# Optimization experiments

Measured on AMD Instinct MI355X. Metric: run time of the kernel, lower is better.

## Reference

```python
import jax, jax.numpy as jnp
import numpy as np
from jax import lax

B = 65536

def _conv3(x, w, b):
    # x: [B,Cin,H,W], w: [Cout,Cin,3,3] (OIHW), SAME padding, stride 1
    y = lax.conv_general_dilated(x, w, (1, 1), 'SAME',
                                 dimension_numbers=('NCHW', 'OIHW', 'NCHW'))
    return y + b[None, :, None, None]

def _gru_cell(x, h, wu, bu, wr, br, wo, bo):
    s = jnp.concatenate([x, h], axis=1)
    update = jax.nn.sigmoid(_conv3(s, wu, bu))
    reset = jax.nn.sigmoid(_conv3(s, wr, br))
    out = jnp.tanh(_conv3(jnp.concatenate([x, h * reset], axis=1), wo, bo))
    return h * (1.0 - update) + out * update

def _mk_cell_params(key, cin, ch):
    ks = jax.random.split(key, 6)
    fan = (cin + ch) * 9
    sc = 1.0 / np.sqrt(fan)
    p = {}
    for i, g in enumerate(['u', 'r', 'o']):
        p['w' + g] = jax.random.normal(ks[2 * i], (ch, cin + ch, 3, 3), jnp.float32) * sc
        p['b' + g] = jax.random.normal(ks[2 * i + 1], (ch,), jnp.float32) * sc
    return p

def setup_inputs() -> dict:
    key = jax.random.key(0)
    k_in, k1, k2, k3, kd1, kd2 = jax.random.split(key, 6)
    inputs = jax.random.normal(k_in, (B, 1, 3, 3), jnp.float32)
    p1 = _mk_cell_params(k1, 1, 32)
    p2 = _mk_cell_params(k2, 32, 64)
    p3 = _mk_cell_params(k3, 64, 16)
    wd = jax.random.normal(kd1, (9, 16 * 3 * 3), jnp.float32) * (1.0 / 12.0)
    bd = jax.random.normal(kd2, (9,), jnp.float32) * (1.0 / 12.0)
    out = {'inputs': inputs, 'wd': wd, 'bd': bd}
    for i, p in enumerate([p1, p2, p3], start=1):
        for k, v in p.items():
            out[f'{k[0]}{i}{k[1]}'] = v  # e.g. w1u, b1u
    return out

def reference(inputs, wd, bd,
              w1u, b1u, w1r, b1r, w1o, b1o,
              w2u, b2u, w2r, b2r, w2o, b2o,
              w3u, b3u, w3r, b3r, w3o, b3o):
    b = inputs.shape[0]
    h1 = jnp.zeros((b, 32, 3, 3), inputs.dtype)
    h2 = jnp.zeros((b, 64, 3, 3), inputs.dtype)
    h3 = jnp.zeros((b, 16, 3, 3), inputs.dtype)
    x1 = _gru_cell(inputs, h1, w1u, b1u, w1r, b1r, w1o, b1o)
    x2 = _gru_cell(x1, h2, w2u, b2u, w2r, b2r, w2o, b2o)
    x3 = _gru_cell(x2, h3, w3u, b3u, w3r, b3r, w3o, b3o)
    out = x3.reshape(b, -1) @ wd.T + bd
    return (out, x1, x2, x3)
```

## Files before the change

### kernel.cpp

```cpp
#include <hip/hip_runtime.h>

#define BATCH 65536

typedef __attribute__((ext_vector_type(8))) short bf16x8;
typedef __attribute__((ext_vector_type(4))) float f32x4;

__device__ __forceinline__ unsigned short f2bf(float f) {
  unsigned int u = __float_as_uint(f);
  u += 0x7fffu + ((u >> 16) & 1u);
  return (unsigned short)(u >> 16);
}
__device__ __forceinline__ unsigned pack_trunc(float lo, float hi) {
  return __builtin_amdgcn_perm(__float_as_uint(hi), __float_as_uint(lo), 0x07060302u);
}

__device__ __forceinline__ float gru_act(float u, float o) {
  u = fmaxf(u, -60.0f);
  o = fmaxf(o, -30.0f);
  float a  = __expf(-u);
  float a2 = __expf(-2.0f * o);
  return (1.0f - a2) * __builtin_amdgcn_rcpf((1.0f + a) * (1.0f + a2));
}

__device__ __forceinline__ float conv_tap(const float* __restrict__ w, int co, int ci,
                                          int p, int q, int CINTOT) {
  int pi = p / 3, pj = p % 3, qi = q / 3, qj = q % 3;
  int di = qi - pi + 1, dj = qj - pj + 1;
  if ((unsigned)di < 3u && (unsigned)dj < 3u)
    return w[((co * CINTOT + ci) * 3 + di) * 3 + dj];
  return 0.0f;
}

__global__ void build_bt(const float* __restrict__ wu, const float* __restrict__ wo,
                         unsigned short* __restrict__ BT, int COUT, int CINX, int CINTOT) {
  int NG = COUT * 9, K = CINX * 9;
  int total = 2 * NG * K;
  int e = blockIdx.x * 256 + threadIdx.x;
  if (e >= total) return;
  int g = e / (NG * K);
  int rem = e - g * (NG * K);
  int n = rem / K, k = rem - n * K;
  BT[e] = f2bf(conv_tap(g ? wo : wu, n / 9, k / 9, n % 9, k % 9, CINTOT));
}

__global__ void build_a1(const float* __restrict__ wu, const float* __restrict__ wo,
                         float* __restrict__ A1) {
  int e = blockIdx.x * 256 + threadIdx.x;
  if (e >= 5184) return;
  int g = e / 2592;
  int rem = e - g * 2592;
  int q = rem / 288, c = rem - q * 288;
  A1[e] = conv_tap(g ? wo : wu, c / 9, 0, c % 9, q, 33);
}

#define OFF_X1L 0
#define OFF_X3L 0
#define OFF_WL 20480
#define OFF_BLB 25664
#define OFF_BL 40960
#define OFF_XL 65536
#define OFF_AL 65536
#define SMEM_BYTES 69632

__global__ __launch_bounds__(512, 4) void megafused(
    const float* __restrict__ xin, const float* __restrict__ A1,
    const float* __restrict__ b1u, const float* __restrict__ b1o,
    const unsigned short* __restrict__ BT2,
    const float* __restrict__ b2u, const float* __restrict__ b2o,
    const unsigned short* __restrict__ BT3,
    const float* __restrict__ b3u, const float* __restrict__ b3o,
    const float* __restrict__ wd, const float* __restrict__ bd,
    float* __restrict__ x1, float* __restrict__ x2,
    float* __restrict__ x3, float* __restrict__ out) {
  __shared__ __align__(16) char smem[SMEM_BYTES];
  char* x1l = smem + OFF_X1L;
  char* Bl = smem + OFF_BL;
  char* Al = smem + OFF_AL;
  unsigned short* x3l = (unsigned short*)(smem + OFF_X3L);
  float* xl = (float*)(smem + OFF_XL);
  float* wl = (float*)(smem + OFF_WL);
  float* blb = (float*)(smem + OFF_BLB);

  const int tid = threadIdx.x;
  const int lane = tid & 63;
  const int wid = tid >> 6;
  const int lrow = lane & 15;
  const int jc = (lane >> 4) & 3;
  const int mh = wid >> 2;
  const int cg = wid & 3;
  const int r0 = blockIdx.x * 64;
  const int srow = tid >> 2, spart = tid & 3;

  unsigned toffB2[3];
  char* wB2[3];
#pragma unroll
  for (int ci = 0; ci < 3; ++ci) {
    int row = ci * 128 + srow;
    int bg = (row < 192) ? row : (384 + row);
    toffB2[ci] = (unsigned)bg * 288u + spart * 8;
    wB2[ci] = Bl + row * 64 + ((spart ^ ((row >> 1) & 3)) << 4);
  }

  for (int c = tid; c < 576; c += 512) xl[(c / 9) * 12 + (c % 9)] = xin[(size_t)r0 * 9 + c];
  __syncthreads();

  bf16x8 pf[3];
#pragma unroll
  for (int ci = 0; ci < 3; ++ci) pf[ci] = *(const bf16x8*)(BT2 + toffB2[ci]);

  for (int uu = 0; uu < 3; ++uu) {
    int u = tid + (uu << 9);
    if (u < 1152) {
      int c = u >> 2, rq = u & 3;
      float au[9], ao[9];
#pragma unroll
      for (int q = 0; q < 9; ++q) {
        au[q] = A1[q * 288 + c];
        ao[q] = A1[2592 + q * 288 + c];
      }
      float bU = b1u[c / 9], bO = b1o[c / 9];
      const int cbase = c >> 3, cb = (c & 7) * 2;
#pragma unroll 4
      for (int i = 0; i < 16; ++i) {
        int r = (rq << 4) + i;
        const float4 xv0 = *(const float4*)&xl[r * 12];
        const float4 xv1 = *(const float4*)&xl[r * 12 + 4];
        const float x8 = xl[r * 12 + 8];
        float uacc = bU, oacc = bO;
        uacc = fmaf(au[0], xv0.x, uacc); oacc = fmaf(ao[0], xv0.x, oacc);
        uacc = fmaf(au[1], xv0.y, uacc); oacc = fmaf(ao[1], xv0.y, oacc);
        uacc = fmaf(au[2], xv0.z, uacc); oacc = fmaf(ao[2], xv0.z, oacc);
        uacc = fmaf(au[3], xv0.w, uacc); oacc = fmaf(ao[3], xv0.w, oacc);
        uacc = fmaf(au[4], xv1.x, uacc); oacc = fmaf(ao[4], xv1.x, oacc);
        uacc = fmaf(au[5], xv1.y, uacc); oacc = fmaf(ao[5], xv1.y, oacc);
        uacc = fmaf(au[6], xv1.z, uacc); oacc = fmaf(ao[6], xv1.z, oacc);
        uacc = fmaf(au[7], xv1.w, uacc); oacc = fmaf(ao[7], xv1.w, oacc);
        uacc = fmaf(au[8], x8, uacc);    oacc = fmaf(ao[8], x8, oacc);
        float v = gru_act(uacc, oacc);
        x1[(size_t)(r0 + r) * 288 + c] = v;
        *(unsigned short*)(x1l + r * 640 + ((cbase ^ (r & 7)) << 4) + cb) =
            (unsigned short)(__float_as_uint(v) >> 16);
      }
    }
  }

  {
    const char* rB[2][3];
#pragma unroll
    for (int g = 0; g < 2; ++g)
#pragma unroll
      for (int f = 0; f < 3; ++f) {
        int rb = g * 192 + (cg * 3 + f) * 16 + lrow;
        rB[g][f] = Bl + rb * 64 + ((jc ^ ((rb >> 1) & 3)) << 4);
      }
    const char* aBase[2];
    int aXor[2];
#pragma unroll
    for (int m = 0; m < 2; ++m) {
      int row = mh * 32 + m * 16 + lrow;
      aBase[m] = x1l + row * 640;
      aXor[m] = row & 7;
    }

    f32x4 acc[2][2][3] = {};
    for (int s = 0; s < 27; ++s) {
      const int kt = s - (s / 9) * 9;
#pragma unroll
      for (int ci = 0; ci < 3; ++ci) *(bf16x8*)wB2[ci] = pf[ci];
      __syncthreads();
      if (s < 26) {
        int ns = s + 1;
        unsigned uoff = (unsigned)(ns / 9) * 55296u + (unsigned)(ns % 9) * 32u;
#pragma unroll
        for (int ci = 0; ci < 3; ++ci)
          pf[ci] = *(const bf16x8*)(BT2 + uoff + toffB2[ci]);
      }
      bf16x8 af[2];
      const int c8 = kt * 4 + jc;
#pragma unroll
      for (int m = 0; m < 2; ++m)
        af[m] = *(const bf16x8*)(aBase[m] + ((c8 ^ aXor[m]) << 4));
      bf16x8 bfr[2][3];
#pragma unroll
      for (int g = 0; g < 2; ++g)
#pragma unroll
        for (int f = 0; f < 3; ++f) bfr[g][f] = *(const bf16x8*)rB[g][f];
#pragma unroll
      for (int m = 0; m < 2; ++m)
#pragma unroll
        for (int g = 0; g < 2; ++g)
#pragma unroll
          for (int f = 0; f < 3; ++f)
            acc[m][g][f] = __builtin_amdgcn_mfma_f32_16x16x32_bf16(
                af[m], bfr[g][f], acc[m][g][f], 0, 0, 0);
      if (kt == 8) {
        const int n0 = (s / 9) * 192;
#pragma unroll
        for (int m = 0; m < 2; ++m)
#pragma unroll
          for (int f = 0; f < 3; ++f) {
            int n = n0 + (cg * 3 + f) * 16 + lrow;
            float bU = b2u[n / 9], bO = b2o[n / 9];
            f32x4 u = acc[m][0][f], o = acc[m][1][f];
#pragma unroll
            for (int t = 0; t < 4; ++t) {
              int r = r0 + mh * 32 + m * 16 + jc * 4 + t;
              x2[(size_t)r * 576 + n] = gru_act(u[t] + bU, o[t] + bO);
            }
            acc[m][0][f] = (f32x4){0.f, 0.f, 0.f, 0.f};
            acc[m][1][f] = (f32x4){0.f, 0.f, 0.f, 0.f};
          }
      }
      __syncthreads();
    }
  }

  {
    unsigned toffB3[3];
    char* wB3[3];
    bool vB3[3];
#pragma unroll
    for (int ci = 0; ci < 3; ++ci) {
      int row = ci * 128 + srow;
      int g = row >= 192;
      int nloc = row - (g ? 192 : 0);
      vB3[ci] = (nloc < 144);
      toffB3[ci] = (unsigned)((g ? 144 : 0) + nloc) * 576u + spart * 8;
      wB3[ci] = Bl + row * 64 + ((spart ^ ((row >> 1) & 3)) << 4);
    }
    const float* pA = x2 + (size_t)(r0 + (tid >> 2)) * 576 + spart * 8;
    char* wAl = Al + (tid >> 2) * 64 + ((spart ^ (((tid >> 2) >> 1) & 3)) << 4);

    float4 pa0 = {}, pa1 = {};
    if (tid < 256) {
      pa0 = *(const float4*)pA;
      pa1 = *(const float4*)(pA + 4);
    }
    bf16x8 pb[3];
#pragma unroll
    for (int ci = 0; ci < 3; ++ci)
      pb[ci] = vB3[ci] ? *(const bf16x8*)(BT3 + toffB3[ci])
                       : (bf16x8){0, 0, 0, 0, 0, 0, 0, 0};

    for (int c = tid; c < 1296; c += 512) wl[c] = wd[c];
    if (tid < 9) blb[tid] = bd[tid];

    const char* rB3[2][3];
#pragma unroll
    for (int g = 0; g < 2; ++g)
#pragma unroll
      for (int f = 0; f < 3; ++f) {
        int rb = g * 192 + (cg * 3 + f) * 16 + lrow;
        rB3[g][f] = Bl + rb * 64 + ((jc ^ ((rb >> 1) & 3)) << 4);
      }
    const char* rA3[2];
#pragma unroll
    for (int m = 0; m < 2; ++m) {
      int row = mh * 32 + m * 16 + lrow;
      rA3[m] = Al + row * 64 + ((jc ^ ((row >> 1) & 3)) << 4);
    }

    f32x4 acc[2][2][3] = {};
    for (int kt = 0; kt < 18; ++kt) {
      if (tid < 256) {
        uint4 h;
        h.x = pack_trunc(pa0.x, pa0.y);
        h.y = pack_trunc(pa0.z, pa0.w);
        h.z = pack_trunc(pa1.x, pa1.y);
        h.w = pack_trunc(pa1.z, pa1.w);
        *(uint4*)wAl = h;
      }
#pragma unroll
      for (int ci = 0; ci < 3; ++ci) *(bf16x8*)wB3[ci] = pb[ci];
      __syncthreads();
      if (kt < 17) {
        if (tid < 256) {
          const float* gp = pA + (kt + 1) * 32;
          pa0 = *(const float4*)gp;
          pa1 = *(const float4*)(gp + 4);
        }
        unsigned uoff = (unsigned)(kt + 1) * 32u;
#pragma unroll
        for (int ci = 0; ci < 3; ++ci)
          if (vB3[ci]) pb[ci] = *(const bf16x8*)(BT3 + uoff + toffB3[ci]);
      }
      bf16x8 af[2];
#pragma unroll
      for (int m = 0; m < 2; ++m) af[m] = *(const bf16x8*)rA3[m];
      bf16x8 bfr[2][3];
#pragma unroll
      for (int g = 0; g < 2; ++g)
#pragma unroll
        for (int f = 0; f < 3; ++f) bfr[g][f] = *(const bf16x8*)rB3[g][f];
#pragma unroll
      for (int m = 0; m < 2; ++m)
#pragma unroll
        for (int g = 0; g < 2; ++g)
#pragma unroll
          for (int f = 0; f < 3; ++f)
            acc[m][g][f] = __builtin_amdgcn_mfma_f32_16x16x32_bf16(
                af[m], bfr[g][f], acc[m][g][f], 0, 0, 0);
      __syncthreads();
    }
    if (cg < 3) {
#pragma unroll
      for (int m = 0; m < 2; ++m)
#pragma unroll
        for (int f = 0; f < 3; ++f) {
          int n = (cg * 3 + f) * 16 + lrow;
          float bU = b3u[n / 9], bO = b3o[n / 9];
          f32x4 u = acc[m][0][f], o = acc[m][1][f];
#pragma unroll
          for (int t = 0; t < 4; ++t) {
            int r = mh * 32 + m * 16 + jc * 4 + t;
            float v = gru_act(u[t] + bU, o[t] + bO);
            x3[(size_t)(r0 + r) * 144 + n] = v;
            x3l[r * 146 + n] = (unsigned short)(__float_as_uint(v) >> 16);
          }
        }
    }
  }
  __syncthreads();

  {
    int row = lane;
    int j = wid;
    float s = blb[j];
    for (int k = 0; k < 144; k += 2) {
      unsigned pr = *(const unsigned*)&x3l[row * 146 + k];
      float v0 = __uint_as_float(pr << 16);
      float v1 = __uint_as_float(pr & 0xffff0000u);
      const float2 w0 = *(const float2*)&wl[j * 144 + k];
      s = fmaf(v0, w0.x, s);
      s = fmaf(v1, w0.y, s);
    }
    out[(size_t)(r0 + row) * 9 + j] = s;
    if (tid < 64) {
      float s8 = blb[8];
      for (int k = 0; k < 144; k += 2) {
        unsigned pr = *(const unsigned*)&x3l[row * 146 + k];
        float v0 = __uint_as_float(pr << 16);
        float v1 = __uint_as_float(pr & 0xffff0000u);
        const float2 w0 = *(const float2*)&wl[8 * 144 + k];
        s8 = fmaf(v0, w0.x, s8);
        s8 = fmaf(v1, w0.y, s8);
      }
      out[(size_t)(r0 + row) * 9 + 8] = s8;
    }
  }
}

extern "C" void kernel_launch(void* const* d_in, const int* in_sizes, int n_in,
                              void* d_out, int out_size, void* d_ws, size_t ws_size,
                              hipStream_t stream) {
  const float* inputs = (const float*)d_in[0];
  const float* wd  = (const float*)d_in[1];
  const float* bd  = (const float*)d_in[2];
  const float* w1u = (const float*)d_in[3];
  const float* b1u = (const float*)d_in[4];
  const float* w1o = (const float*)d_in[7];
  const float* b1o = (const float*)d_in[8];
  const float* w2u = (const float*)d_in[9];
  const float* b2u = (const float*)d_in[10];
  const float* w2o = (const float*)d_in[13];
  const float* b2o = (const float*)d_in[14];
  const float* w3u = (const float*)d_in[15];
  const float* b3u = (const float*)d_in[16];
  const float* w3o = (const float*)d_in[19];
  const float* b3o = (const float*)d_in[20];

  float* out = (float*)d_out;
  float* x1 = out + (size_t)BATCH * 9;
  float* x2 = x1 + (size_t)BATCH * 288;
  float* x3 = x2 + (size_t)BATCH * 576;

  unsigned short* BT2 = (unsigned short*)d_ws;
  unsigned short* BT3 = BT2 + 331776;
  float* A1 = (float*)((char*)d_ws + 995328);

  build_bt<<<1296, 256, 0, stream>>>(w2u, w2o, BT2, 64, 32, 96);
  build_bt<<<648, 256, 0, stream>>>(w3u, w3o, BT3, 16, 64, 80);
  build_a1<<<21, 256, 0, stream>>>(w1u, w1o, A1);

  megafused<<<BATCH / 64, 512, 0, stream>>>(inputs, A1, b1u, b1o, BT2, b2u, b2o,
                                            BT3, b3u, b3o, wd, bd, x1, x2, x3, out);
}
```

Measured before the change: 163.5 us.

## Double-buffer LDS tiles for layer 2/3 GEMMs with one barrier per step

Splits the weight and activation LDS tiles into two buffers, so the next k-step's tile is written while the current one is consumed. This drops one of the two __syncthreads per iteration, replacing it with a custom s_waitcnt plus s_barrier, and prefetches global data two steps ahead. LDS use grows to about 100KB, so launch bounds fall from 4 to 2 blocks per CU, which cuts occupancy and latency hiding. The layer-1 input row stride also changes from 12 to 13 floats, which alters the LDS bank mapping for those loads.

```diff
diff --git a/kernel.cpp b/kernel.cpp
--- a/kernel.cpp
+++ b/kernel.cpp
@@ -20,6 +20,13 @@
   float a  = __expf(-u);
   float a2 = __expf(-2.0f * o);
   return (1.0f - a2) * __builtin_amdgcn_rcpf((1.0f + a) * (1.0f + a2));
+}
+
+__device__ __forceinline__ void bar_lds() {
+  asm volatile("s_waitcnt lgkmcnt(0)" ::: "memory");
+  __builtin_amdgcn_sched_barrier(0);
+  __builtin_amdgcn_s_barrier();
+  __builtin_amdgcn_sched_barrier(0);
 }
 
 __device__ __forceinline__ float conv_tap(const float* __restrict__ w, int co, int ci,
@@ -58,11 +65,13 @@
 #define OFF_WL 20480
 #define OFF_BLB 25664
 #define OFF_BL 40960
-#define OFF_XL 65536
-#define OFF_AL 65536
-#define SMEM_BYTES 69632
-
-__global__ __launch_bounds__(512, 4) void megafused(
+#define BL_STRIDE 24576
+#define OFF_AL 90112
+#define AL_STRIDE 4096
+#define OFF_XL 98304
+#define SMEM_BYTES 101632
+
+__global__ __launch_bounds__(512, 2) void megafused(
     const float* __restrict__ xin, const float* __restrict__ A1,
     const float* __restrict__ b1u, const float* __restrict__ b1o,
     const unsigned short* __restrict__ BT2,
@@ -92,16 +101,16 @@
   const int srow = tid >> 2, spart = tid & 3;
 
   unsigned toffB2[3];
-  char* wB2[3];
+  int wOffB2[3];
 #pragma unroll
   for (int ci = 0; ci < 3; ++ci) {
     int row = ci * 128 + srow;
     int bg = (row < 192) ? row : (384 + row);
     toffB2[ci] = (unsigned)bg * 288u + spart * 8;
-    wB2[ci] = Bl + row * 64 + ((spart ^ ((row >> 1) & 3)) << 4);
+    wOffB2[ci] = row * 64 + ((spart ^ ((row >> 1) & 3)) << 4);
   }
 
-  for (int c = tid; c < 576; c += 512) xl[(c / 9) * 12 + (c % 9)] = xin[(size_t)r0 * 9 + c];
+  for (int c = tid; c < 576; c += 512) xl[(c / 9) * 13 + (c % 9)] = xin[(size_t)r0 * 9 + c];
   __syncthreads();
 
   bf16x8 pf[3];
@@ -123,9 +132,9 @@
 #pragma unroll 4
       for (int i = 0; i < 16; ++i) {
         int r = (rq << 4) + i;
-        const float4 xv0 = *(const float4*)&xl[r * 12];
-        const float4 xv1 = *(const float4*)&xl[r * 12 + 4];
-        const float x8 = xl[r * 12 + 8];
+        const float4 xv0 = *(const float4*)&xl[r * 13];
+        const float4 xv1 = *(const float4*)&xl[r * 13 + 4];
+        const float x8 = xl[r * 13 + 8];
         float uacc = bU, oacc = bO;
         uacc = fmaf(au[0], xv0.x, uacc); oacc = fmaf(ao[0], xv0.x, oacc);
         uacc = fmaf(au[1], xv0.y, uacc); oacc = fmaf(ao[1], xv0.y, oacc);
@@ -145,13 +154,13 @@
   }
 
   {
-    const char* rB[2][3];
+    int rBoff[2][3];
 #pragma unroll
     for (int g = 0; g < 2; ++g)
 #pragma unroll
       for (int f = 0; f < 3; ++f) {
         int rb = g * 192 + (cg * 3 + f) * 16 + lrow;
-        rB[g][f] = Bl + rb * 64 + ((jc ^ ((rb >> 1) & 3)) << 4);
+        rBoff[g][f] = rb * 64 + ((jc ^ ((rb >> 1) & 3)) << 4);
       }
     const char* aBase[2];
     int aXor[2];
@@ -162,19 +171,16 @@
       aXor[m] = row & 7;
     }
 
+#pragma unroll
+    for (int ci = 0; ci < 3; ++ci) *(bf16x8*)(Bl + wOffB2[ci]) = pf[ci];
+#pragma unroll
+    for (int ci = 0; ci < 3; ++ci) pf[ci] = *(const bf16x8*)(BT2 + 32u + toffB2[ci]);
+    bar_lds();
+
     f32x4 acc[2][2][3] = {};
     for (int s = 0; s < 27; ++s) {
       const int kt = s - (s / 9) * 9;
-#pragma unroll
-      for (int ci = 0; ci < 3; ++ci) *(bf16x8*)wB2[ci] = pf[ci];
-      __syncthreads();
-      if (s < 26) {
-        int ns = s + 1;
-        unsigned uoff = (unsigned)(ns / 9) * 55296u + (unsigned)(ns % 9) * 32u;
-#pragma unroll
-        for (int ci = 0; ci < 3; ++ci)
-          pf[ci] = *(const bf16x8*)(BT2 + uoff + toffB2[ci]);
-      }
+      const int bsel = (s & 1) * BL_STRIDE;
       bf16x8 af[2];
       const int c8 = kt * 4 + jc;
 #pragma unroll
@@ -184,7 +190,8 @@
 #pragma unroll
       for (int g = 0; g < 2; ++g)
 #pragma unroll
-        for (int f = 0; f < 3; ++f) bfr[g][f] = *(const bf16x8*)rB[g][f];
+        for (int f = 0; f < 3; ++f)
+          bfr[g][f] = *(const bf16x8*)(Bl + bsel + rBoff[g][f]);
 #pragma unroll
       for (int m = 0; m < 2; ++m)
 #pragma unroll
@@ -211,13 +218,27 @@
             acc[m][1][f] = (f32x4){0.f, 0.f, 0.f, 0.f};
           }
       }
-      __syncthreads();
+      if (s < 26) {
+        const int wsel = ((s + 1) & 1) * BL_STRIDE;
+#pragma unroll
+        for (int ci = 0; ci < 3; ++ci)
+          *(bf16x8*)(Bl + wsel + wOffB2[ci]) = pf[ci];
+        if (s < 25) {
+          int ns = s + 2;
+          unsigned uoff = (unsigned)(ns / 9) * 55296u + (unsigned)(ns % 9) * 32u;
+#pragma unroll
+          for (int ci = 0; ci < 3; ++ci)
+            pf[ci] = *(const bf16x8*)(BT2 + uoff + toffB2[ci]);
+        }
+        bar_lds();
+      }
     }
   }
+  __syncthreads();
 
   {
     unsigned toffB3[3];
-    char* wB3[3];
+    int wOffB3[3];
     bool vB3[3];
 #pragma unroll
     for (int ci = 0; ci < 3; ++ci) {
@@ -226,10 +247,10 @@
       int nloc = row - (g ? 192 : 0);
       vB3[ci] = (nloc < 144);
       toffB3[ci] = (unsigned)((g ? 144 : 0) + nloc) * 576u + spart * 8;
-      wB3[ci] = Bl + row * 64 + ((spart ^ ((row >> 1) & 3)) << 4);
+      wOffB3[ci] = row * 64 + ((spart ^ ((row >> 1) & 3)) << 4);
     }
     const float* pA = x2 + (size_t)(r0 + (tid >> 2)) * 576 + spart * 8;
-    char* wAl = Al + (tid >> 2) * 64 + ((spart ^ (((tid >> 2) >> 1) & 3)) << 4);
+    const int wAloff = (tid >> 2) * 64 + ((spart ^ (((tid >> 2) >> 1) & 3)) << 4);
 
     float4 pa0 = {}, pa1 = {};
     if (tid < 256) {
@@ -245,53 +266,53 @@
     for (int c = tid; c < 1296; c += 512) wl[c] = wd[c];
     if (tid < 9) blb[tid] = bd[tid];
 
-    const char* rB3[2][3];
+    int rBoff3[2][3];
 #pragma unroll
     for (int g = 0; g < 2; ++g)
 #pragma unroll
       for (int f = 0; f < 3; ++f) {
         int rb = g * 192 + (cg * 3 + f) * 16 + lrow;
-        rB3[g][f] = Bl + rb * 64 + ((jc ^ ((rb >> 1) & 3)) << 4);
-      }
-    const char* rA3[2];
+        rBoff3[g][f] = rb * 64 + ((jc ^ ((rb >> 1) & 3)) << 4);
+      }
+    int rAoff3[2];
 #pragma unroll
     for (int m = 0; m < 2; ++m) {
       int row = mh * 32 + m * 16 + lrow;
-      rA3[m] = Al + row * 64 + ((jc ^ ((row >> 1) & 3)) << 4);
-    }
+      rAoff3[m] = row * 64 + ((jc ^ ((row >> 1) & 3)) << 4);
+    }
+
+    if (tid < 256) {
+      uint4 h;
+      h.x = pack_trunc(pa0.x, pa0.y);
+      h.y = pack_trunc(pa0.z, pa0.w);
+      h.z = pack_trunc(pa1.x, pa1.y);
+      h.w = pack_trunc(pa1.z, pa1.w);
+      *(uint4*)(Al + wAloff) = h;
+    }
+#pragma unroll
+    for (int ci = 0; ci < 3; ++ci) *(bf16x8*)(Bl + wOffB3[ci]) = pb[ci];
+    if (tid < 256) {
+      pa0 = *(const float4*)(pA + 32);
+      pa1 = *(const float4*)(pA + 36);
+    }
+#pragma unroll
+    for (int ci = 0; ci < 3; ++ci)
+      if (vB3[ci]) pb[ci] = *(const bf16x8*)(BT3 + 32u + toffB3[ci]);
+    bar_lds();
 
     f32x4 acc[2][2][3] = {};
     for (int kt = 0; kt < 18; ++kt) {
-      if (tid < 256) {
-        uint4 h;
-        h.x = pack_trunc(pa0.x, pa0.y);
-        h.y = pack_trunc(pa0.z, pa0.w);
-        h.z = pack_trunc(pa1.x, pa1.y);
-        h.w = pack_trunc(pa1.z, pa1.w);
-        *(uint4*)wAl = h;
-      }
-#pragma unroll
-      for (int ci = 0; ci < 3; ++ci) *(bf16x8*)wB3[ci] = pb[ci];
-      __syncthreads();
-      if (kt < 17) {
-        if (tid < 256) {
-          const float* gp = pA + (kt + 1) * 32;
-          pa0 = *(const float4*)gp;
-          pa1 = *(const float4*)(gp + 4);
-        }
-        unsigned uoff = (unsigned)(kt + 1) * 32u;
-#pragma unroll
-        for (int ci = 0; ci < 3; ++ci)
-          if (vB3[ci]) pb[ci] = *(const bf16x8*)(BT3 + uoff + toffB3[ci]);
-      }
+      const int bsel = (kt & 1) * BL_STRIDE;
+      const int asel = (kt & 1) * AL_STRIDE;
       bf16x8 af[2];
 #pragma unroll
-      for (int m = 0; m < 2; ++m) af[m] = *(const bf16x8*)rA3[m];
+      for (int m = 0; m < 2; ++m) af[m] = *(const bf16x8*)(Al + asel + rAoff3[m]);
       bf16x8 bfr[2][3];
 #pragma unroll
       for (int g = 0; g < 2; ++g)
 #pragma unroll
-        for (int f = 0; f < 3; ++f) bfr[g][f] = *(const bf16x8*)rB3[g][f];
+        for (int f = 0; f < 3; ++f)
+          bfr[g][f] = *(const bf16x8*)(Bl + bsel + rBoff3[g][f]);
 #pragma unroll
       for (int m = 0; m < 2; ++m)
 #pragma unroll
@@ -300,7 +321,33 @@
           for (int f = 0; f < 3; ++f)
             acc[m][g][f] = __builtin_amdgcn_mfma_f32_16x16x32_bf16(
                 af[m], bfr[g][f], acc[m][g][f], 0, 0, 0);
-      __syncthreads();
+      if (kt < 17) {
+        const int wbsel = ((kt + 1) & 1) * BL_STRIDE;
+        const int wasel = ((kt + 1) & 1) * AL_STRIDE;
+        if (tid < 256) {
+          uint4 h;
+          h.x = pack_trunc(pa0.x, pa0.y);
+          h.y = pack_trunc(pa0.z, pa0.w);
+          h.z = pack_trunc(pa1.x, pa1.y);
+          h.w = pack_trunc(pa1.z, pa1.w);
+          *(uint4*)(Al + wasel + wAloff) = h;
+        }
+#pragma unroll
+        for (int ci = 0; ci < 3; ++ci)
+          *(bf16x8*)(Bl + wbsel + wOffB3[ci]) = pb[ci];
+        if (kt < 16) {
+          if (tid < 256) {
+            const float* gp = pA + (kt + 2) * 32;
+            pa0 = *(const float4*)gp;
+            pa1 = *(const float4*)(gp + 4);
+          }
+          unsigned uoff = (unsigned)(kt + 2) * 32u;
+#pragma unroll
+          for (int ci = 0; ci < 3; ++ci)
+            if (vB3[ci]) pb[ci] = *(const bf16x8*)(BT3 + uoff + toffB3[ci]);
+        }
+        bar_lds();
+      }
     }
     if (cg < 3) {
 #pragma unroll
```

Measured after the change: 217.1 us. 32.8% more time.

## Load GEMM weight fragments directly from global into registers, dropping LDS staging

Applied to the files above, without the earlier changes.

Layer-2 and layer-3 MFMA loops no longer stage B weight tiles through shared memory. Each wave now loads its own bf16 fragments straight from global into a double-buffered register set, and layer 3 reads and packs its x2 A-operand directly from global. This removes the two __syncthreads per k-step and shrinks shared memory from about 68 KB to about 43 KB, which may allow more resident blocks; the xl row stride also changes to 13 to avoid bank conflicts. The cost is redundant global/L2 traffic, since waves sharing a column group each fetch the same weights, and more register pressure from the double buffers and full unrolling.

```diff
diff --git a/kernel.cpp b/kernel.cpp
--- a/kernel.cpp
+++ b/kernel.cpp
@@ -57,10 +57,8 @@
 #define OFF_X3L 0
 #define OFF_WL 20480
 #define OFF_BLB 25664
-#define OFF_BL 40960
-#define OFF_XL 65536
-#define OFF_AL 65536
-#define SMEM_BYTES 69632
+#define OFF_XL 40960
+#define SMEM_BYTES 44288
 
 __global__ __launch_bounds__(512, 4) void megafused(
     const float* __restrict__ xin, const float* __restrict__ A1,
@@ -74,8 +72,6 @@
     float* __restrict__ x3, float* __restrict__ out) {
   __shared__ __align__(16) char smem[SMEM_BYTES];
   char* x1l = smem + OFF_X1L;
-  char* Bl = smem + OFF_BL;
-  char* Al = smem + OFF_AL;
   unsigned short* x3l = (unsigned short*)(smem + OFF_X3L);
   float* xl = (float*)(smem + OFF_XL);
   float* wl = (float*)(smem + OFF_WL);
@@ -89,24 +85,22 @@
   const int mh = wid >> 2;
   const int cg = wid & 3;
   const int r0 = blockIdx.x * 64;
-  const int srow = tid >> 2, spart = tid & 3;
-
-  unsigned toffB2[3];
-  char* wB2[3];
-#pragma unroll
-  for (int ci = 0; ci < 3; ++ci) {
-    int row = ci * 128 + srow;
-    int bg = (row < 192) ? row : (384 + row);
-    toffB2[ci] = (unsigned)bg * 288u + spart * 8;
-    wB2[ci] = Bl + row * 64 + ((spart ^ ((row >> 1) & 3)) << 4);
-  }
-
-  for (int c = tid; c < 576; c += 512) xl[(c / 9) * 12 + (c % 9)] = xin[(size_t)r0 * 9 + c];
+
+  unsigned bvoff[3];
+#pragma unroll
+  for (int f = 0; f < 3; ++f)
+    bvoff[f] = (unsigned)(((cg * 3 + f) * 16 + lrow) * 576 + jc * 16);
+  const char* BT2b = (const char*)BT2;
+
+  for (int c = tid; c < 576; c += 512) xl[(c / 9) * 13 + (c % 9)] = xin[(size_t)r0 * 9 + c];
   __syncthreads();
 
-  bf16x8 pf[3];
-#pragma unroll
-  for (int ci = 0; ci < 3; ++ci) pf[ci] = *(const bf16x8*)(BT2 + toffB2[ci]);
+  bf16x8 bA[2][3], bB[2][3];
+#pragma unroll
+  for (int g = 0; g < 2; ++g)
+#pragma unroll
+    for (int f = 0; f < 3; ++f)
+      bA[g][f] = *(const bf16x8*)(BT2b + g * 331776u + bvoff[f]);
 
   for (int uu = 0; uu < 3; ++uu) {
     int u = tid + (uu << 9);
@@ -123,9 +117,9 @@
 #pragma unroll 4
       for (int i = 0; i < 16; ++i) {
         int r = (rq << 4) + i;
-        const float4 xv0 = *(const float4*)&xl[r * 12];
-        const float4 xv1 = *(const float4*)&xl[r * 12 + 4];
-        const float x8 = xl[r * 12 + 8];
+        const float4 xv0 = *(const float4*)&xl[r * 13];
+        const float4 xv1 = *(const float4*)&xl[r * 13 + 4];
+        const float x8 = xl[r * 13 + 8];
         float uacc = bU, oacc = bO;
         uacc = fmaf(au[0], xv0.x, uacc); oacc = fmaf(ao[0], xv0.x, oacc);
         uacc = fmaf(au[1], xv0.y, uacc); oacc = fmaf(ao[1], xv0.y, oacc);
@@ -143,16 +137,9 @@
       }
     }
   }
+  __syncthreads();
 
   {
-    const char* rB[2][3];
-#pragma unroll
-    for (int g = 0; g < 2; ++g)
-#pragma unroll
-      for (int f = 0; f < 3; ++f) {
-        int rb = g * 192 + (cg * 3 + f) * 16 + lrow;
-        rB[g][f] = Bl + rb * 64 + ((jc ^ ((rb >> 1) & 3)) << 4);
-      }
     const char* aBase[2];
     int aXor[2];
 #pragma unroll
@@ -163,28 +150,22 @@
     }
 
     f32x4 acc[2][2][3] = {};
-    for (int s = 0; s < 27; ++s) {
-      const int kt = s - (s / 9) * 9;
-#pragma unroll
-      for (int ci = 0; ci < 3; ++ci) *(bf16x8*)wB2[ci] = pf[ci];
-      __syncthreads();
+    auto step = [&](int s, bf16x8 (&cur)[2][3], bf16x8 (&nxt)[2][3]) {
+      const int kt = s % 9, nch = s / 9;
       if (s < 26) {
-        int ns = s + 1;
-        unsigned uoff = (unsigned)(ns / 9) * 55296u + (unsigned)(ns % 9) * 32u;
-#pragma unroll
-        for (int ci = 0; ci < 3; ++ci)
-          pf[ci] = *(const bf16x8*)(BT2 + uoff + toffB2[ci]);
+        const unsigned uoff =
+            (unsigned)((s + 1) / 9) * 110592u + (unsigned)((s + 1) % 9) * 64u;
+#pragma unroll
+        for (int g = 0; g < 2; ++g)
+#pragma unroll
+          for (int f = 0; f < 3; ++f)
+            nxt[g][f] = *(const bf16x8*)(BT2b + uoff + g * 331776u + bvoff[f]);
       }
       bf16x8 af[2];
       const int c8 = kt * 4 + jc;
 #pragma unroll
       for (int m = 0; m < 2; ++m)
         af[m] = *(const bf16x8*)(aBase[m] + ((c8 ^ aXor[m]) << 4));
-      bf16x8 bfr[2][3];
-#pragma unroll
-      for (int g = 0; g < 2; ++g)
-#pragma unroll
-        for (int f = 0; f < 3; ++f) bfr[g][f] = *(const bf16x8*)rB[g][f];
 #pragma unroll
       for (int m = 0; m < 2; ++m)
 #pragma unroll
@@ -192,106 +173,75 @@
 #pragma unroll
           for (int f = 0; f < 3; ++f)
             acc[m][g][f] = __builtin_amdgcn_mfma_f32_16x16x32_bf16(
-                af[m], bfr[g][f], acc[m][g][f], 0, 0, 0);
+                af[m], cur[g][f], acc[m][g][f], 0, 0, 0);
       if (kt == 8) {
-        const int n0 = (s / 9) * 192;
+        const int n0 = nch * 192;
 #pragma unroll
         for (int m = 0; m < 2; ++m)
 #pragma unroll
           for (int f = 0; f < 3; ++f) {
             int n = n0 + (cg * 3 + f) * 16 + lrow;
             float bU = b2u[n / 9], bO = b2o[n / 9];
-            f32x4 u = acc[m][0][f], o = acc[m][1][f];
+            f32x4 uv = acc[m][0][f], ov = acc[m][1][f];
 #pragma unroll
             for (int t = 0; t < 4; ++t) {
               int r = r0 + mh * 32 + m * 16 + jc * 4 + t;
-              x2[(size_t)r * 576 + n] = gru_act(u[t] + bU, o[t] + bO);
+              x2[(size_t)r * 576 + n] = gru_act(uv[t] + bU, ov[t] + bO);
             }
             acc[m][0][f] = (f32x4){0.f, 0.f, 0.f, 0.f};
             acc[m][1][f] = (f32x4){0.f, 0.f, 0.f, 0.f};
           }
       }
-      __syncthreads();
+    };
+#pragma unroll
+    for (int s = 0; s < 27; ++s) {
+      if (s & 1) step(s, bB, bA);
+      else       step(s, bA, bB);
     }
   }
+  __syncthreads();
+
+  for (int c = tid; c < 1296; c += 512) wl[c] = wd[c];
+  if (tid < 9) blb[tid] = bd[tid];
 
   {
-    unsigned toffB3[3];
-    char* wB3[3];
-    bool vB3[3];
-#pragma unroll
-    for (int ci = 0; ci < 3; ++ci) {
-      int row = ci * 128 + srow;
-      int g = row >= 192;
-      int nloc = row - (g ? 192 : 0);
-      vB3[ci] = (nloc < 144);
-      toffB3[ci] = (unsigned)((g ? 144 : 0) + nloc) * 576u + spart * 8;
-      wB3[ci] = Bl + row * 64 + ((spart ^ ((row >> 1) & 3)) << 4);
-    }
-    const float* pA = x2 + (size_t)(r0 + (tid >> 2)) * 576 + spart * 8;
-    char* wAl = Al + (tid >> 2) * 64 + ((spart ^ (((tid >> 2) >> 1) & 3)) << 4);
-
-    float4 pa0 = {}, pa1 = {};
-    if (tid < 256) {
-      pa0 = *(const float4*)pA;
-      pa1 = *(const float4*)(pA + 4);
-    }
-    bf16x8 pb[3];
-#pragma unroll
-    for (int ci = 0; ci < 3; ++ci)
-      pb[ci] = vB3[ci] ? *(const bf16x8*)(BT3 + toffB3[ci])
-                       : (bf16x8){0, 0, 0, 0, 0, 0, 0, 0};
-
-    for (int c = tid; c < 1296; c += 512) wl[c] = wd[c];
-    if (tid < 9) blb[tid] = bd[tid];
-
-    const char* rB3[2][3];
-#pragma unroll
-    for (int g = 0; g < 2; ++g)
-#pragma unroll
-      for (int f = 0; f < 3; ++f) {
-        int rb = g * 192 + (cg * 3 + f) * 16 + lrow;
-        rB3[g][f] = Bl + rb * 64 + ((jc ^ ((rb >> 1) & 3)) << 4);
-      }
-    const char* rA3[2];
-#pragma unroll
-    for (int m = 0; m < 2; ++m) {
-      int row = mh * 32 + m * 16 + lrow;
-      rA3[m] = Al + row * 64 + ((jc ^ ((row >> 1) & 3)) << 4);
-    }
+    unsigned bvoff3[3];
+#pragma unroll
+    for (int f = 0; f < 3; ++f) {
+      int nr = (cg * 3 + f) * 16 + lrow;
+      if (cg == 3) nr -= 64;
+      bvoff3[f] = (unsigned)(nr * 1152 + jc * 16);
+    }
+    const char* BT3b = (const char*)BT3;
+    unsigned avoff[2];
+#pragma unroll
+    for (int m = 0; m < 2; ++m)
+      avoff[m] = (unsigned)(((mh * 32 + m * 16 + lrow) * 576 + jc * 8) * 4);
+    const char* x2b = (const char*)(x2 + (size_t)r0 * 576);
 
     f32x4 acc[2][2][3] = {};
+#pragma unroll
     for (int kt = 0; kt < 18; ++kt) {
-      if (tid < 256) {
-        uint4 h;
-        h.x = pack_trunc(pa0.x, pa0.y);
-        h.y = pack_trunc(pa0.z, pa0.w);
-        h.z = pack_trunc(pa1.x, pa1.y);
-        h.w = pack_trunc(pa1.z, pa1.w);
-        *(uint4*)wAl = h;
-      }
-#pragma unroll
-      for (int ci = 0; ci < 3; ++ci) *(bf16x8*)wB3[ci] = pb[ci];
-      __syncthreads();
-      if (kt < 17) {
-        if (tid < 256) {
-          const float* gp = pA + (kt + 1) * 32;
-          pa0 = *(const float4*)gp;
-          pa1 = *(const float4*)(gp + 4);
-        }
-        unsigned uoff = (unsigned)(kt + 1) * 32u;
-#pragma unroll
-        for (int ci = 0; ci < 3; ++ci)
-          if (vB3[ci]) pb[ci] = *(const bf16x8*)(BT3 + uoff + toffB3[ci]);
-      }
+      bf16x8 bfr[2][3];
+      const unsigned uB = (unsigned)kt * 64u;
+#pragma unroll
+      for (int g = 0; g < 2; ++g)
+#pragma unroll
+        for (int f = 0; f < 3; ++f)
+          bfr[g][f] = *(const bf16x8*)(BT3b + uB + g * 165888u + bvoff3[f]);
       bf16x8 af[2];
-#pragma unroll
-      for (int m = 0; m < 2; ++m) af[m] = *(const bf16x8*)rA3[m];
-      bf16x8 bfr[2][3];
-#pragma unroll
-      for (int g = 0; g < 2; ++g)
-#pragma unroll
-        for (int f = 0; f < 3; ++f) bfr[g][f] = *(const bf16x8*)rB3[g][f];
+      const unsigned uA = (unsigned)kt * 128u;
+#pragma unroll
+      for (int m = 0; m < 2; ++m) {
+        float4 a0 = *(const float4*)(x2b + avoff[m] + uA);
+        float4 a1 = *(const float4*)(x2b + avoff[m] + uA + 16);
+        union { uint4 u; bf16x8 v; } cv;
+        cv.u.x = pack_trunc(a0.x, a0.y);
+        cv.u.y = pack_trunc(a0.z, a0.w);
+        cv.u.z = pack_trunc(a1.x, a1.y);
+        cv.u.w = pack_trunc(a1.z, a1.w);
+        af[m] = cv.v;
+      }
 #pragma unroll
       for (int m = 0; m < 2; ++m)
 #pragma unroll
@@ -300,7 +250,6 @@
           for (int f = 0; f < 3; ++f)
             acc[m][g][f] = __builtin_amdgcn_mfma_f32_16x16x32_bf16(
                 af[m], bfr[g][f], acc[m][g][f], 0, 0, 0);
-      __syncthreads();
     }
     if (cg < 3) {
 #pragma unroll
@@ -309,11 +258,11 @@
         for (int f = 0; f < 3; ++f) {
           int n = (cg * 3 + f) * 16 + lrow;
           float bU = b3u[n / 9], bO = b3o[n / 9];
-          f32x4 u = acc[m][0][f], o = acc[m][1][f];
+          f32x4 uv = acc[m][0][f], ov = acc[m][1][f];
 #pragma unroll
           for (int t = 0; t < 4; ++t) {
             int r = mh * 32 + m * 16 + jc * 4 + t;
-            float v = gru_act(u[t] + bU, o[t] + bO);
+            float v = gru_act(uv[t] + bU, ov[t] + bO);
             x3[(size_t)(r0 + r) * 144 + n] = v;
             x3l[r * 146 + n] = (unsigned short)(__float_as_uint(v) >> 16);
           }
```

New measurement: 393.7 us. +140.8%, slower.
